# Performance work log

Measured on AMD Instinct MI355X. Metric: run time of the kernel, lower is better.

The kernel has to match this reference:

```python
import jax, jax.numpy as jnp
import numpy as np

ROPE_THETA = 10000.0

def _rope(t):
    # t: (B, S, H, D) -- rotate-half RoPE over last dim
    B, S, H, D = t.shape
    inv_freq = 1.0 / (ROPE_THETA ** (jnp.arange(0, D, 2, dtype=jnp.float32) / D))  # (D/2,)
    ang = jnp.arange(S, dtype=jnp.float32)[:, None] * inv_freq[None, :]            # (S, D/2)
    cos = jnp.concatenate([jnp.cos(ang), jnp.cos(ang)], axis=-1)[None, :, None, :] # (1,S,1,D)
    sin = jnp.concatenate([jnp.sin(ang), jnp.sin(ang)], axis=-1)[None, :, None, :]
    t1, t2 = jnp.split(t, 2, axis=-1)
    rot = jnp.concatenate([-t2, t1], axis=-1)
    return t * cos.astype(t.dtype) + rot * sin.astype(t.dtype)

def setup_inputs() -> dict:
    key = jax.random.key(0)
    kx, kq, kk, kv, ko = jax.random.split(key, 5)
    B, S, DIM = 2, 2048, 2048
    x = jax.random.normal(kx, (B, S, DIM), dtype=jnp.float32)
    mask = jnp.tril(jnp.ones((S, S), dtype=bool))[None, None, :, :]  # causal (1,1,S,S)
    scale = DIM ** -0.5
    wq = jax.random.normal(kq, (DIM, DIM), dtype=jnp.float32) * scale
    wk = jax.random.normal(kk, (DIM, DIM), dtype=jnp.float32) * scale
    wv = jax.random.normal(kv, (DIM, DIM), dtype=jnp.float32) * scale
    wo = jax.random.normal(ko, (DIM, DIM), dtype=jnp.float32) * scale
    return {"x": x, "mask": mask, "wq": wq, "wk": wk, "wv": wv, "wo": wo}

def reference(x, mask, wq, wk, wv, wo):
    B, S, DIM = x.shape
    H = 16
    D = DIM // H
    scale = D ** -0.5
    # nn.Linear: y = x @ W.T
    q = (x @ wq.T).reshape(B, S, H, D)
    k = (x @ wk.T).reshape(B, S, H, D)
    v = (x @ wv.T).reshape(B, S, H, D)
    q = _rope(q)
    k = _rope(k)
    scores = jnp.einsum('bqhd,bkhd->bhqk', q, k) * scale
    scores = jnp.where(mask, scores, -jnp.inf)
    attn = jax.nn.softmax(scores, axis=-1)
    out = jnp.einsum('bhqk,bkhd->bqhd', attn, v).reshape(B, S, DIM)
    return out @ wo.T
```

## Files before the change

### kernel.cpp

```cpp
#include <hip/hip_runtime.h>
#include <cstdint>

typedef unsigned short u16;
typedef uint32_t u32;
typedef __attribute__((ext_vector_type(8))) short bf16x8;
typedef __attribute__((ext_vector_type(4))) float f32x4;
typedef __attribute__((ext_vector_type(16))) float f32x16;

#define DIM_ 2048
#define S_   2048
#define B_   2
#define H_   16
#define HD_  128
#define M_   (B_ * S_)

__device__ __forceinline__ u16 f2b(float f) {
  union { float f; uint32_t u; } v; v.f = f;
  uint32_t u = v.u;
  return (u16)((u + 0x7FFFu + ((u >> 16) & 1u)) >> 16);
}
__device__ __forceinline__ float b2f(u16 h) {
  union { uint32_t u; float f; } v; v.u = ((uint32_t)h) << 16;
  return v.f;
}

__device__ __forceinline__ u32 cvtpk(float lo, float hi) {
  u32 r;
  asm("v_cvt_pk_bf16_f32 %0, %1, %2" : "=v"(r) : "v"(lo), "v"(hi));
  return r;
}

typedef __attribute__((address_space(3))) u16 lds_u16_t;
typedef __attribute__((address_space(1))) const u16 glob_u16_t;

__device__ __forceinline__ void gload16(const u16* g, u16* l) {
  __builtin_amdgcn_global_load_lds((glob_u16_t*)g, (lds_u16_t*)l, 16, 0, 0);
}

__global__ void convert5_kernel(const float* __restrict__ x, const float* __restrict__ wq,
                                const float* __restrict__ wk, const float* __restrict__ wv,
                                const float* __restrict__ wo, u16* __restrict__ xb,
                                u16* __restrict__ wqb, u16* __restrict__ wkb,
                                u16* __restrict__ wvb, u16* __restrict__ wob) {
  const float* src;
  u16* dst;
  int n;
  switch (blockIdx.y) {
    case 0: src = x;  dst = xb;  n = M_ * DIM_;   break;
    case 1: src = wq; dst = wqb; n = DIM_ * DIM_; break;
    case 2: src = wk; dst = wkb; n = DIM_ * DIM_; break;
    case 3: src = wv; dst = wvb; n = DIM_ * DIM_; break;
    default: src = wo; dst = wob; n = DIM_ * DIM_; break;
  }
  int i = (blockIdx.x * blockDim.x + threadIdx.x) * 4;
  const int stride = gridDim.x * blockDim.x * 4;
  for (; i < n; i += stride) {
    float4 v = *reinterpret_cast<const float4*>(src + i);
    uint64_t p = (uint64_t)f2b(v.x) | ((uint64_t)f2b(v.y) << 16) |
                 ((uint64_t)f2b(v.z) << 32) | ((uint64_t)f2b(v.w) << 48);
    *reinterpret_cast<uint64_t*>(dst + i) = p;
  }
}

__global__ void rope_table_kernel(float* __restrict__ cosT, float* __restrict__ sinT) {
  int i = blockIdx.x * blockDim.x + threadIdx.x;
  if (i >= S_ * 64) return;
  int s = i >> 6, d = i & 63;
  float inv = powf(10000.0f, -(float)d * (1.0f / 64.0f));
  float ang = (float)s * inv;
  cosT[i] = cosf(ang);
  sinT[i] = sinf(ang);
}

__global__ void rope_apply_kernel(u16* __restrict__ qb, u16* __restrict__ kb,
                                  const float* __restrict__ cosT,
                                  const float* __restrict__ sinT) {
  u16* buf = blockIdx.y ? kb : qb;
  int i = blockIdx.x * blockDim.x + threadIdx.x;
  if (i >= B_ * S_ * H_ * 64) return;
  int d = i & 63;
  int h = (i >> 6) & (H_ - 1);
  int row = i >> 10;
  int s = row & (S_ - 1);
  u16* p = buf + (size_t)row * DIM_ + h * HD_ + d;
  float t1 = b2f(p[0]);
  float t2 = b2f(p[64]);
  float c = cosT[s * 64 + d];
  float sn = sinT[s * 64 + d];
  p[0]  = f2b(t1 * c - t2 * sn);
  p[64] = f2b(t2 * c + t1 * sn);
}

#define NT_ 32

template <bool OUTF32>
__device__ __forceinline__ void gemm256x128_body(const u16* __restrict__ A,
                                                 const u16* __restrict__ W, int mt, int nt,
                                                 u16* __restrict__ Cb, float* __restrict__ Cf) {
  __shared__ __align__(16) u16 lds[49152];
  const int tid = threadIdx.x;
  const int lane = tid & 63;
  const int w = tid >> 6;
  const int wm = w >> 2, wn = w & 3;
  const int l15 = lane & 15, lg = lane >> 4;

  const u16* Ab = A + (size_t)(mt * 256) * DIM_;
  const u16* Bb = W + (size_t)(nt * 128) * DIM_;

  f32x4 acc[8][2];
#pragma unroll
  for (int i = 0; i < 8; ++i)
#pragma unroll
    for (int j = 0; j < 2; ++j) acc[i][j] = (f32x4){0.f, 0.f, 0.f, 0.f};

  auto stageA = [&](int buf, int half, int kt) {
#pragma unroll
    for (int s = 0; s < 2; ++s) {
      const int cb = s * 512 + w * 64;
      const int i = cb + lane;
      const int r = half * 128 + (i >> 3);
      const int c = (i & 7) ^ (r & 7);
      gload16(Ab + (size_t)r * DIM_ + kt * 64 + c * 8,
              lds + buf * 24576 + half * 8192 + cb * 8);
    }
  };
  auto stageB = [&](int buf, int kt) {
#pragma unroll
    for (int s = 0; s < 2; ++s) {
      const int cb = s * 512 + w * 64;
      const int i = cb + lane;
      const int r = i >> 3;
      const int c = (i & 7) ^ (r & 7);
      gload16(Bb + (size_t)r * DIM_ + kt * 64 + c * 8,
              lds + buf * 24576 + 16384 + cb * 8);
    }
  };
  auto rdA = [&](int buf, int mh, int mi, int ks) -> bf16x8 {
    const int row = wm * 128 + mh * 64 + mi * 16 + l15;
    const int chunk = ((ks << 2) + lg) ^ (l15 & 7);
    return *(const bf16x8*)(lds + buf * 24576 + row * 64 + chunk * 8);
  };
  auto rdB = [&](int buf, int ni, int ks) -> bf16x8 {
    const int row = wn * 32 + ni * 16 + l15;
    const int chunk = ((ks << 2) + lg) ^ (l15 & 7);
    return *(const bf16x8*)(lds + buf * 24576 + 16384 + row * 64 + chunk * 8);
  };

  bf16x8 a[8], b[4];

  auto phase0 = [&](int t, int cur, bool stg, int wv) {
#pragma unroll
    for (int ni = 0; ni < 2; ++ni)
#pragma unroll
      for (int ks = 0; ks < 2; ++ks) b[ni * 2 + ks] = rdB(cur, ni, ks);
#pragma unroll
    for (int mi = 0; mi < 4; ++mi)
#pragma unroll
      for (int ks = 0; ks < 2; ++ks) a[mi * 2 + ks] = rdA(cur, 0, mi, ks);
    if (stg) stageA(cur ^ 1, 1, t + 1);
    __builtin_amdgcn_s_barrier();
    asm volatile("s_waitcnt lgkmcnt(0)" ::: "memory");
    __builtin_amdgcn_sched_barrier(0);
    __builtin_amdgcn_s_setprio(1);
#pragma unroll
    for (int mi = 0; mi < 4; ++mi)
#pragma unroll
      for (int ni = 0; ni < 2; ++ni)
#pragma unroll
        for (int ks = 0; ks < 2; ++ks)
          acc[mi][ni] = __builtin_amdgcn_mfma_f32_16x16x32_bf16(a[mi * 2 + ks],
                                                                b[ni * 2 + ks],
                                                                acc[mi][ni], 0, 0, 0);
    __builtin_amdgcn_s_setprio(0);
    __builtin_amdgcn_sched_barrier(0);
    if (wv == 6) asm volatile("s_waitcnt vmcnt(6)" ::: "memory");
    else         asm volatile("s_waitcnt vmcnt(0)" ::: "memory");
    __builtin_amdgcn_sched_barrier(0);
    __builtin_amdgcn_s_barrier();
  };
  auto phase1 = [&](int t, int cur, bool stg, int wv) {
#pragma unroll
    for (int mi = 0; mi < 4; ++mi)
#pragma unroll
      for (int ks = 0; ks < 2; ++ks) a[mi * 2 + ks] = rdA(cur, 1, mi, ks);
    if (stg) { stageB(cur, t + 2); stageA(cur, 0, t + 2); }
    __builtin_amdgcn_s_barrier();
    asm volatile("s_waitcnt lgkmcnt(0)" ::: "memory");
    __builtin_amdgcn_sched_barrier(0);
    __builtin_amdgcn_s_setprio(1);
#pragma unroll
    for (int mi = 0; mi < 4; ++mi)
#pragma unroll
      for (int ni = 0; ni < 2; ++ni)
#pragma unroll
        for (int ks = 0; ks < 2; ++ks)
          acc[4 + mi][ni] = __builtin_amdgcn_mfma_f32_16x16x32_bf16(a[mi * 2 + ks],
                                                                    b[ni * 2 + ks],
                                                                    acc[4 + mi][ni], 0, 0, 0);
    __builtin_amdgcn_s_setprio(0);
    if (wv >= 0) {
      __builtin_amdgcn_sched_barrier(0);
      if (wv == 6)      asm volatile("s_waitcnt vmcnt(6)" ::: "memory");
      else if (wv == 2) asm volatile("s_waitcnt vmcnt(2)" ::: "memory");
      else              asm volatile("s_waitcnt vmcnt(0)" ::: "memory");
      __builtin_amdgcn_sched_barrier(0);
      __builtin_amdgcn_s_barrier();
    }
  };

  stageA(0, 0, 0);
  stageA(0, 1, 0);
  stageB(0, 0);
  stageA(1, 0, 1);
  stageB(1, 1);
  __builtin_amdgcn_sched_barrier(0);
  asm volatile("s_waitcnt vmcnt(4)" ::: "memory");
  __builtin_amdgcn_sched_barrier(0);
  __builtin_amdgcn_s_barrier();

  for (int t = 0; t < NT_ - 2; ++t) {
    const int cur = t & 1;
    phase0(t, cur, true, 6);
    phase1(t, cur, true, 6);
  }
  phase0(NT_ - 2, (NT_ - 2) & 1, true, 6);
  phase1(NT_ - 2, (NT_ - 2) & 1, false, 2);
  phase0(NT_ - 1, (NT_ - 1) & 1, false, 0);
  phase1(NT_ - 1, (NT_ - 1) & 1, false, -1);

#pragma unroll
  for (int mi = 0; mi < 8; ++mi)
#pragma unroll
    for (int ni = 0; ni < 2; ++ni) {
      const int row = mt * 256 + wm * 128 + mi * 16 + lg * 4;
      const int col = nt * 128 + wn * 32 + ni * 16 + l15;
#pragma unroll
      for (int r = 0; r < 4; ++r) {
        if (OUTF32)
          Cf[(size_t)(row + r) * DIM_ + col] = acc[mi][ni][r];
        else
          Cb[(size_t)(row + r) * DIM_ + col] = f2b(acc[mi][ni][r]);
      }
    }
}

__global__ __launch_bounds__(512, 2) void gemm8_qkv_kernel(
    const u16* __restrict__ xb, const u16* __restrict__ wqb, const u16* __restrict__ wkb,
    const u16* __restrict__ wvb, u16* __restrict__ qb, u16* __restrict__ kb,
    u16* __restrict__ vb) {
  const int bid = blockIdx.x;
  const int logical = (bid & 7) * 96 + (bid >> 3);
  const int mt = logical / 48;
  const int rem = logical % 48;
  const int z = rem >> 4;
  const int nt = rem & 15;
  const u16* W = (z == 0) ? wqb : (z == 1) ? wkb : wvb;
  u16* out = (z == 0) ? qb : (z == 1) ? kb : vb;
  gemm256x128_body<false>(xb, W, mt, nt, out, nullptr);
}

__global__ __launch_bounds__(512, 2) void gemm8_out_kernel(const u16* __restrict__ aob,
                                                           const u16* __restrict__ wob,
                                                           float* __restrict__ C) {
  const int bid = blockIdx.x;
  const int logical = (bid & 7) * 32 + (bid >> 3);
  const int mt = logical >> 4;
  const int nt = logical & 15;
  gemm256x128_body<true>(aob, wob, mt, nt, nullptr, C);
}

#define CEXP 0.12751744f

__global__ __launch_bounds__(256, 2) void attn_kernel(const u16* __restrict__ q,
                                                      const u16* __restrict__ k,
                                                      const u16* __restrict__ v,
                                                      u16* __restrict__ ao) {
  __shared__ __align__(16) u16 smem[17408];
  u16* kTl = smem;
  u16* vTl = smem + 8192;

  const int qt   = blockIdx.z ? (int)blockIdx.x : (int)(gridDim.x - 1 - blockIdx.x);
  const int head = blockIdx.y;
  const int b    = blockIdx.z;
  const int t = threadIdx.x;
  const int lane = t & 63;
  const int w = t >> 6;
  const int l31 = lane & 31;
  const int hi = lane >> 5;
  const int kxor = (lane & 7) << 3;
  const int qrow0 = qt * 128 + w * 32;
  const size_t bS = (size_t)b * S_;

  bf16x8 qf[8];
  {
    const u16* qrow = q + (bS + qrow0 + l31) * DIM_ + head * HD_;
#pragma unroll
    for (int st = 0; st < 8; ++st)
      qf[st] = *(const bf16x8*)(qrow + st * 16 + hi * 8);
  }

  f32x16 accO[4];
#pragma unroll
  for (int db = 0; db < 4; ++db)
#pragma unroll
    for (int r = 0; r < 16; ++r) accO[db][r] = 0.f;
  float m = -1e30f, l = 0.f;

  const int tmax_w = 2 * qt + (w >> 1);
  const int ttend = 2 * qt + 1;

  for (int tt = 0; tt <= ttend; ++tt) {
    __syncthreads();

    bf16x8 vv[4];
#pragma unroll
    for (int p = 0; p < 4; ++p) {
      const int dchunk = p * 4 + w;
      vv[p] = *(const bf16x8*)(v + (bS + tt * 64 + lane) * DIM_ + head * HD_ + dchunk * 8);
    }
#pragma unroll
    for (int p = 0; p < 4; ++p) {
      const int cb = p * 256 + w * 64;
      const int cid = cb + lane;
      const int kr = cid >> 4;
      const int cg = (cid & 15) ^ (kr & 7);
      gload16(k + (bS + tt * 64 + kr) * DIM_ + head * HD_ + cg * 8, kTl + cb * 8);
    }
#pragma unroll
    for (int p = 0; p < 4; ++p) {
      const int dchunk = p * 4 + w;
#pragma unroll
      for (int j = 0; j < 8; ++j) {
        const int d = dchunk * 8 + j;
        vTl[d * 64 + (lane ^ ((d & 7) << 3))] = (u16)vv[p][j];
      }
    }
    __syncthreads();

    if (tt <= tmax_w) {
      f32x16 sA, sB;
#pragma unroll
      for (int r = 0; r < 16; ++r) { sA[r] = 0.f; sB[r] = 0.f; }
      __builtin_amdgcn_s_setprio(1);
#pragma unroll
      for (int st = 0; st < 8; ++st) {
        const int dc = st * 16 + hi * 8;
        bf16x8 k0 = *(const bf16x8*)(kTl + l31 * 128 + (dc ^ kxor));
        bf16x8 k1 = *(const bf16x8*)(kTl + (32 + l31) * 128 + (dc ^ kxor));
        sA = __builtin_amdgcn_mfma_f32_32x32x16_bf16(k0, qf[st], sA, 0, 0, 0);
        sB = __builtin_amdgcn_mfma_f32_32x32x16_bf16(k1, qf[st], sB, 0, 0, 0);
      }
      __builtin_amdgcn_s_setprio(0);

      const int qg = qrow0 + l31;
      if (tt * 64 + 63 > qrow0) {
        const int kb = tt * 64 + 4 * hi;
#pragma unroll
        for (int r = 0; r < 16; ++r) {
          const int kg = kb + (r & 3) + 8 * (r >> 2);
          sA[r] = (kg <= qg) ? sA[r] : -1e30f;
          sB[r] = (kg + 32 <= qg) ? sB[r] : -1e30f;
        }
      }

      float mx[8];
#pragma unroll
      for (int i = 0; i < 8; ++i)
        mx[i] = fmaxf(fmaxf(sA[i], sA[i + 8]), fmaxf(sB[i], sB[i + 8]));
#pragma unroll
      for (int i = 0; i < 4; ++i) mx[i] = fmaxf(mx[i], mx[i + 4]);
      float pm = fmaxf(fmaxf(mx[0], mx[1]), fmaxf(mx[2], mx[3]));
      pm = fmaxf(pm, __shfl_xor(pm, 32));
      const float mN = fmaxf(m, pm);
      if (!__all(pm - m <= 90.5f)) {
        const float osc = exp2f((m - mN) * CEXP);
        l *= osc;
#pragma unroll
        for (int db = 0; db < 4; ++db)
#pragma unroll
          for (int r = 0; r < 16; ++r) accO[db][r] *= osc;
        m = mN;
      }
      const float mc = m * CEXP;
      float lsv[4] = {0.f, 0.f, 0.f, 0.f};
#pragma unroll
      for (int r = 0; r < 16; ++r) {
        const float pa = exp2f(__builtin_fmaf(sA[r], CEXP, -mc));
        const float pb = exp2f(__builtin_fmaf(sB[r], CEXP, -mc));
        sA[r] = pa; sB[r] = pb;
        lsv[r & 3] += pa + pb;
      }
      float ls = (lsv[0] + lsv[1]) + (lsv[2] + lsv[3]);
      ls += __shfl_xor(ls, 32);
      l += ls;

#define PV_STEP(ARR, R0, ST2)                                                      \
      {                                                                            \
        u32 a0 = cvtpk(ARR[(R0) + 0], ARR[(R0) + 1]);                              \
        u32 a1 = cvtpk(ARR[(R0) + 2], ARR[(R0) + 3]);                              \
        u32 b0 = cvtpk(ARR[(R0) + 4], ARR[(R0) + 5]);                              \
        u32 b1 = cvtpk(ARR[(R0) + 6], ARR[(R0) + 7]);                              \
        asm("v_permlane32_swap_b32 %0, %1" : "+v"(a0), "+v"(b0));                  \
        asm("v_permlane32_swap_b32 %0, %1" : "+v"(a1), "+v"(b1));                  \
        union { u32 uu[4]; bf16x8 v8; } pf;                                        \
        pf.uu[0] = a0; pf.uu[1] = a1; pf.uu[2] = b0; pf.uu[3] = b1;                \
        const int ko = (ST2) * 16 + hi * 8;                                        \
        __builtin_amdgcn_s_setprio(1);                                             \
        _Pragma("unroll")                                                          \
        for (int db = 0; db < 4; ++db) {                                           \
          const int dr = db * 32 + l31;                                            \
          bf16x8 vf = *(const bf16x8*)(vTl + dr * 64 + (ko ^ kxor));               \
          accO[db] =                                                               \
              __builtin_amdgcn_mfma_f32_32x32x16_bf16(vf, pf.v8, accO[db], 0, 0, 0); \
        }                                                                          \
        __builtin_amdgcn_s_setprio(0);                                             \
      }
      PV_STEP(sA, 0, 0)
      PV_STEP(sA, 8, 1)
      PV_STEP(sB, 0, 2)
      PV_STEP(sB, 8, 3)
#undef PV_STEP
    }
  }

  __syncthreads();
  const float linv = 1.0f / l;
  u16* oT = smem + w * 4352;
#pragma unroll
  for (int db = 0; db < 4; ++db)
#pragma unroll
    for (int q4 = 0; q4 < 4; ++q4) {
      const int dbase = db * 32 + q4 * 8 + hi * 4;
      const u32 lo = cvtpk(accO[db][q4 * 4 + 0] * linv, accO[db][q4 * 4 + 1] * linv);
      const u32 hiw = cvtpk(accO[db][q4 * 4 + 2] * linv, accO[db][q4 * 4 + 3] * linv);
      *(u32*)(oT + l31 * 136 + dbase) = lo;
      *(u32*)(oT + l31 * 136 + dbase + 2) = hiw;
    }
  __syncthreads();
#pragma unroll
  for (int i = 0; i < 8; ++i) {
    const int cid = i * 64 + lane;
    const int qloc = cid >> 4;
    const int c = cid & 15;
    const bf16x8 val = *(const bf16x8*)(oT + qloc * 136 + c * 8);
    *(bf16x8*)(ao + (bS + qrow0 + qloc) * DIM_ + head * HD_ + c * 8) = val;
  }
}

extern "C" void kernel_launch(void* const* d_in, const int* in_sizes, int n_in,
                              void* d_out, int out_size, void* d_ws, size_t ws_size,
                              hipStream_t stream) {
  const float* x  = (const float*)d_in[0];
  const float* wq = (const float*)d_in[2];
  const float* wk = (const float*)d_in[3];
  const float* wv = (const float*)d_in[4];
  const float* wo = (const float*)d_in[5];

  char* ws = (char*)d_ws;
  size_t off = 0;
  auto carve = [&](size_t bytes) { char* p = ws + off; off += bytes; return p; };
  u16* xb   = (u16*)carve((size_t)M_ * DIM_ * 2);
  u16* wqb  = (u16*)carve((size_t)DIM_ * DIM_ * 2);
  u16* wkb  = (u16*)carve((size_t)DIM_ * DIM_ * 2);
  u16* wvb  = (u16*)carve((size_t)DIM_ * DIM_ * 2);
  u16* wob  = (u16*)carve((size_t)DIM_ * DIM_ * 2);
  u16* qb   = (u16*)carve((size_t)M_ * DIM_ * 2);
  u16* kb   = (u16*)carve((size_t)M_ * DIM_ * 2);
  u16* vb   = (u16*)carve((size_t)M_ * DIM_ * 2);
  u16* aob  = (u16*)carve((size_t)M_ * DIM_ * 2);
  float* cosT = (float*)carve((size_t)S_ * 64 * 4);
  float* sinT = (float*)carve((size_t)S_ * 64 * 4);
  if (off > ws_size) return;

  dim3 gc(1024, 5);
  convert5_kernel<<<gc, 256, 0, stream>>>(x, wq, wk, wv, wo, xb, wqb, wkb, wvb, wob);
  rope_table_kernel<<<512, 256, 0, stream>>>(cosT, sinT);

  gemm8_qkv_kernel<<<768, 512, 0, stream>>>(xb, wqb, wkb, wvb, qb, kb, vb);

  dim3 gr((B_ * S_ * H_ * 64) / 256, 2);
  rope_apply_kernel<<<gr, 256, 0, stream>>>(qb, kb, cosT, sinT);

  dim3 ga(S_ / 128, H_, B_);
  attn_kernel<<<ga, 256, 0, stream>>>(qb, kb, vb, aob);

  gemm8_out_kernel<<<256, 512, 0, stream>>>(aob, wob, (float*)d_out);
}
```

Baseline: 283.5 us.

## Replace QKV GEMM with 256x256 tile kernel and macro-scheduled quarter pipeline

Adds a dedicated QKV projection kernel that computes 256x256 output tiles instead of 256x128. It uses a double-buffered LDS layout of 128KB with swizzled addressing. Each k-tile is split into four MFMA quarter phases, interleaved with async global-to-LDS loads for the next tiles under explicit waitcnt, barriers and priority hints. The larger tile halves the grid and raises operand reuse per block. The trade-off is more LDS and registers per block, likely one resident block per CU and an uneven final wave. The output-projection GEMM keeps the old body, with the template parameter removed.

```diff
diff --git a/kernel.cpp b/kernel.cpp
--- a/kernel.cpp
+++ b/kernel.cpp
@@ -36,6 +36,8 @@
 __device__ __forceinline__ void gload16(const u16* g, u16* l) {
   __builtin_amdgcn_global_load_lds((glob_u16_t*)g, (lds_u16_t*)l, 16, 0, 0);
 }
+#define GLD0(SRC, DST) \
+  __builtin_amdgcn_global_load_lds((glob_u16_t*)(SRC), (lds_u16_t*)(DST), 16, 0, 0)
 
 __global__ void convert5_kernel(const float* __restrict__ x, const float* __restrict__ wq,
                                 const float* __restrict__ wk, const float* __restrict__ wv,
@@ -93,11 +95,180 @@
 
 #define NT_ 32
 
-template <bool OUTF32>
-__device__ __forceinline__ void gemm256x128_body(const u16* __restrict__ A,
-                                                 const u16* __restrict__ W, int mt, int nt,
-                                                 u16* __restrict__ Cb, float* __restrict__ Cf) {
+#define STAGE_A(BUF, Q, OFFU) do {                                             \
+    GLD0(sAq##Q##0 + (OFFU), lds + (BUF)*32768 + (Q)*4096 + waA);              \
+    GLD0(sAq##Q##1 + (OFFU), lds + (BUF)*32768 + (Q)*4096 + 8192 + waA);       \
+  } while (0)
+#define STAGE_B(BUF, Q, OFFU) do {                                             \
+    GLD0(sBq##Q##0 + (OFFU), lds + (BUF)*32768 + 16384 + (Q)*2048 + waB);      \
+    GLD0(sBq##Q##1 + (OFFU), lds + (BUF)*32768 + 16384 + 8192 + (Q)*2048 + waB); \
+  } while (0)
+
+#define RD_A(BUF, KS, MH, MI) (*(const bf16x8*)(pA##BUF##k##KS + (MH)*4096 + (MI)*1024))
+#define RD_B(BUF, KS, NH, NI) (*(const bf16x8*)(pB##BUF##k##KS + (NH)*2048 + (NI)*1024))
+
+#define LOAD_A(BUF, MH) do {                                                   \
+    a[0] = RD_A(BUF, 0, MH, 0); a[1] = RD_A(BUF, 1, MH, 0);                    \
+    a[2] = RD_A(BUF, 0, MH, 1); a[3] = RD_A(BUF, 1, MH, 1);                    \
+    a[4] = RD_A(BUF, 0, MH, 2); a[5] = RD_A(BUF, 1, MH, 2);                    \
+    a[6] = RD_A(BUF, 0, MH, 3); a[7] = RD_A(BUF, 1, MH, 3);                    \
+  } while (0)
+#define LOAD_B(BUF, NH) do {                                                   \
+    b[0] = RD_B(BUF, 0, NH, 0); b[1] = RD_B(BUF, 1, NH, 0);                    \
+    b[2] = RD_B(BUF, 0, NH, 1); b[3] = RD_B(BUF, 1, NH, 1);                    \
+  } while (0)
+
+#define MFMA_Q(MB, NB)                                                         \
+  _Pragma("unroll")                                                            \
+  for (int mi = 0; mi < 4; ++mi)                                               \
+    _Pragma("unroll")                                                          \
+    for (int ni = 0; ni < 2; ++ni)                                             \
+      _Pragma("unroll")                                                        \
+      for (int ks = 0; ks < 2; ++ks)                                           \
+        acc[(MB) + mi][(NB) + ni] = __builtin_amdgcn_mfma_f32_16x16x32_bf16(   \
+            a[mi * 2 + ks], b[ni * 2 + ks], acc[(MB) + mi][(NB) + ni], 0, 0, 0);
+
+#define PH(MB, NB)                                                             \
+  __builtin_amdgcn_s_barrier();                                                \
+  asm volatile("s_waitcnt lgkmcnt(0)" ::: "memory");                           \
+  __builtin_amdgcn_sched_barrier(0);                                           \
+  __builtin_amdgcn_s_setprio(1);                                               \
+  MFMA_Q(MB, NB);                                                              \
+  __builtin_amdgcn_s_setprio(0);                                               \
+  __builtin_amdgcn_s_barrier();
+
+#define TILE(T, BUF, NBUF, OFF1, OFF2) do {                                    \
+                                                            \
+    LOAD_A(BUF, 0);                                                            \
+    LOAD_B(BUF, 0);                                                            \
+    if ((T) + 1 < NT_) STAGE_B(NBUF, 0, OFF1);                                 \
+    PH(0, 0)                                                                   \
+                                         \
+    LOAD_B(BUF, 1);                                                            \
+    if ((T) + 2 < NT_) STAGE_A(BUF, 0, OFF2);                                  \
+    PH(0, 2)                                                                   \
+                                                 \
+    LOAD_A(BUF, 1);                                                            \
+    if ((T) + 2 < NT_) STAGE_B(BUF, 1, OFF2);                                  \
+    PH(4, 2)                                                                   \
+     \
+    LOAD_B(BUF, 0);                                                            \
+    if ((T) + 2 < NT_) STAGE_A(BUF, 1, OFF2);                                  \
+    __builtin_amdgcn_s_barrier();                                              \
+    asm volatile("s_waitcnt lgkmcnt(0)" ::: "memory");                         \
+    __builtin_amdgcn_sched_barrier(0);                                         \
+    __builtin_amdgcn_s_setprio(1);                                             \
+    MFMA_Q(4, 0);                                                              \
+    __builtin_amdgcn_s_setprio(0);                                             \
+    __builtin_amdgcn_sched_barrier(0);                                         \
+    if ((T) < NT_ - 2) {                                                       \
+      asm volatile("s_waitcnt vmcnt(6)" ::: "memory");                         \
+    } else if ((T) == NT_ - 2) {                                               \
+      asm volatile("s_waitcnt vmcnt(0)" ::: "memory");                         \
+    }                                                                          \
+    __builtin_amdgcn_sched_barrier(0);                                         \
+    __builtin_amdgcn_s_barrier();                                              \
+  } while (0)
+
+__global__ __launch_bounds__(512, 2) void gemm256_qkv_kernel(
+    const u16* __restrict__ xb, const u16* __restrict__ wqb, const u16* __restrict__ wkb,
+    const u16* __restrict__ wvb, u16* __restrict__ qb, u16* __restrict__ kb,
+    u16* __restrict__ vb) {
+  __shared__ __align__(16) u16 lds[65536];
+
+  const int bid = blockIdx.x;
+  const int logical = (bid & 7) * 48 + (bid >> 3);
+  const int mt = logical / 24;
+  const int rem = logical % 24;
+  const int z = rem >> 3;
+  const int nt = rem & 7;
+  const u16* W = (z == 0) ? wqb : (z == 1) ? wkb : wvb;
+  u16* out = (z == 0) ? qb : (z == 1) ? kb : vb;
+
+  const int tid = threadIdx.x;
+  const int lane = tid & 63;
+  const int w = tid >> 6;
+  const int wm = w >> 2, wn = w & 3;
+  const int l15 = lane & 15, lg = lane >> 4;
+
+  const u16* Ag = xb + (size_t)(mt * 256) * DIM_;
+  const u16* Bg = W + (size_t)(nt * 256) * DIM_;
+
+  const int waA = w * 512;
+  const int waB = (w >> 2) * 4096 + (w & 3) * 512;
+
+  const int csw = ((lane & 7) ^ (lane >> 3)) * 8;
+  const int arb = w * 8 + (lane >> 3);
+  const u16* sAq00 = Ag + (size_t)(arb +   0) * DIM_ + csw;
+  const u16* sAq01 = Ag + (size_t)(arb + 128) * DIM_ + csw;
+  const u16* sAq10 = Ag + (size_t)(arb +  64) * DIM_ + csw;
+  const u16* sAq11 = Ag + (size_t)(arb + 192) * DIM_ + csw;
+  const int brb = (w >> 2) * 64 + (w & 3) * 8 + (lane >> 3);
+  const u16* sBq00 = Bg + (size_t)(brb +   0) * DIM_ + csw;
+  const u16* sBq01 = Bg + (size_t)(brb + 128) * DIM_ + csw;
+  const u16* sBq10 = Bg + (size_t)(brb +  32) * DIM_ + csw;
+  const u16* sBq11 = Bg + (size_t)(brb + 160) * DIM_ + csw;
+
+  const int x7 = l15 & 7;
+  const int lr0 = l15 * 64 + ((lg ^ x7) * 8);
+  const int lr1 = l15 * 64 + (((4 | lg) ^ x7) * 8);
+  const u16* pA0k0 = lds + wm * 8192 + lr0;
+  const u16* pA0k1 = lds + wm * 8192 + lr1;
+  const u16* pA1k0 = pA0k0 + 32768;
+  const u16* pA1k1 = pA0k1 + 32768;
+  const u16* pB0k0 = lds + 16384 + wn * 4096 + lr0;
+  const u16* pB0k1 = lds + 16384 + wn * 4096 + lr1;
+  const u16* pB1k0 = pB0k0 + 32768;
+  const u16* pB1k1 = pB0k1 + 32768;
+
+  f32x4 acc[8][4];
+#pragma unroll
+  for (int i = 0; i < 8; ++i)
+#pragma unroll
+    for (int j = 0; j < 4; ++j) acc[i][j] = (f32x4){0.f, 0.f, 0.f, 0.f};
+
+  bf16x8 a[8], b[4];
+
+  STAGE_A(0, 0, 0);
+  STAGE_B(0, 0, 0);
+  STAGE_A(0, 1, 0);
+  STAGE_B(0, 1, 0);
+  STAGE_A(1, 0, 64);
+  STAGE_B(1, 1, 64);
+  STAGE_A(1, 1, 64);
+  __builtin_amdgcn_sched_barrier(0);
+  asm volatile("s_waitcnt vmcnt(6)" ::: "memory");
+  __builtin_amdgcn_sched_barrier(0);
+  __builtin_amdgcn_s_barrier();
+
+  for (int t = 0; t < NT_; t += 2) {
+    TILE(t, 0, 1, 64, 128);
+    TILE(t + 1, 1, 0, 128, 192);
+    sAq00 += 128; sAq01 += 128; sAq10 += 128; sAq11 += 128;
+    sBq00 += 128; sBq01 += 128; sBq10 += 128; sBq11 += 128;
+  }
+
+#pragma unroll
+  for (int mi = 0; mi < 8; ++mi)
+#pragma unroll
+    for (int ni = 0; ni < 4; ++ni) {
+      const int row = mt * 256 + wm * 128 + mi * 16 + lg * 4;
+      const int col = nt * 256 + wn * 64 + ni * 16 + l15;
+#pragma unroll
+      for (int r = 0; r < 4; ++r)
+        out[(size_t)(row + r) * DIM_ + col] = f2b(acc[mi][ni][r]);
+    }
+}
+
+__global__ __launch_bounds__(512, 2) void gemm8_out_kernel(const u16* __restrict__ A,
+                                                           const u16* __restrict__ W,
+                                                           float* __restrict__ Cf) {
   __shared__ __align__(16) u16 lds[49152];
+  const int bid = blockIdx.x;
+  const int logical = (bid & 7) * 32 + (bid >> 3);
+  const int mt = logical >> 4;
+  const int nt = logical & 15;
+
   const int tid = threadIdx.x;
   const int lane = tid & 63;
   const int w = tid >> 6;
@@ -235,38 +406,9 @@
       const int row = mt * 256 + wm * 128 + mi * 16 + lg * 4;
       const int col = nt * 128 + wn * 32 + ni * 16 + l15;
 #pragma unroll
-      for (int r = 0; r < 4; ++r) {
-        if (OUTF32)
-          Cf[(size_t)(row + r) * DIM_ + col] = acc[mi][ni][r];
-        else
-          Cb[(size_t)(row + r) * DIM_ + col] = f2b(acc[mi][ni][r]);
-      }
-    }
-}
-
-__global__ __launch_bounds__(512, 2) void gemm8_qkv_kernel(
-    const u16* __restrict__ xb, const u16* __restrict__ wqb, const u16* __restrict__ wkb,
-    const u16* __restrict__ wvb, u16* __restrict__ qb, u16* __restrict__ kb,
-    u16* __restrict__ vb) {
-  const int bid = blockIdx.x;
-  const int logical = (bid & 7) * 96 + (bid >> 3);
-  const int mt = logical / 48;
-  const int rem = logical % 48;
-  const int z = rem >> 4;
-  const int nt = rem & 15;
-  const u16* W = (z == 0) ? wqb : (z == 1) ? wkb : wvb;
-  u16* out = (z == 0) ? qb : (z == 1) ? kb : vb;
-  gemm256x128_body<false>(xb, W, mt, nt, out, nullptr);
-}
-
-__global__ __launch_bounds__(512, 2) void gemm8_out_kernel(const u16* __restrict__ aob,
-                                                           const u16* __restrict__ wob,
-                                                           float* __restrict__ C) {
-  const int bid = blockIdx.x;
-  const int logical = (bid & 7) * 32 + (bid >> 3);
-  const int mt = logical >> 4;
-  const int nt = logical & 15;
-  gemm256x128_body<true>(aob, wob, mt, nt, nullptr, C);
+      for (int r = 0; r < 4; ++r)
+        Cf[(size_t)(row + r) * DIM_ + col] = acc[mi][ni][r];
+    }
 }
 
 #define CEXP 0.12751744f
@@ -476,7 +618,7 @@
   convert5_kernel<<<gc, 256, 0, stream>>>(x, wq, wk, wv, wo, xb, wqb, wkb, wvb, wob);
   rope_table_kernel<<<512, 256, 0, stream>>>(cosT, sinT);
 
-  gemm8_qkv_kernel<<<768, 512, 0, stream>>>(xb, wqb, wkb, wvb, qb, kb, vb);
+  gemm256_qkv_kernel<<<384, 512, 0, stream>>>(xb, wqb, wkb, wvb, qb, kb, vb);
 
   dim3 gr((B_ * S_ * H_ * 64) / 256, 2);
   rope_apply_kernel<<<gr, 256, 0, stream>>>(qb, kb, cosT, sinT);
```

New measurement: 286.3 us. About the same (+1.0%).
